# Performance work log

Hardware: AMD Instinct MI355X
Metric: run time of the kernel (lower is better)

Reference implementation:

```python
import jax, jax.numpy as jnp
import numpy as np

V, D, B, L = 100000, 64, 4096, 200

def setup_inputs() -> dict:
    key = jax.random.key(0)
    ks = jax.random.split(key, 10)
    s = 0.05  # keep activations in a sane range for sigmoid
    return {
        "item_ids": jax.random.randint(ks[0], (B,), 0, V),
        "history": jax.random.randint(ks[1], (B, L), 0, V),
        "hist_len": jax.random.randint(ks[2], (B,), 1, L + 1),
        "emb_table": jax.random.normal(ks[3], (V, D), jnp.float32) * s,
        "aW1": jax.random.normal(ks[4], (3 * D, D), jnp.float32) * s,
        "ab1": jnp.zeros((D,), jnp.float32),
        "aW2": jax.random.normal(ks[5], (D, 1), jnp.float32) * s,
        "ab2": jnp.zeros((1,), jnp.float32),
        "fW1": jax.random.normal(ks[6], (3 * D, 128), jnp.float32) * s,
        "fb1": jnp.zeros((128,), jnp.float32),
        "fW2": jax.random.normal(ks[7], (128, 64), jnp.float32) * s,
        "fb2": jnp.zeros((64,), jnp.float32),
        "fW3": jax.random.normal(ks[8], (64, 1), jnp.float32) * s,
        "fb3": jnp.zeros((1,), jnp.float32),
    }

def reference(item_ids, history, hist_len, emb_table, aW1, ab1, aW2, ab2,
              fW1, fb1, fW2, fb2, fW3, fb3):
    target = emb_table[item_ids]                      # [B, D]
    hist = emb_table[history]                         # [B, L, D]
    # original pads short histories with zero rows -> zero the padded tail
    mask = (jnp.arange(hist.shape[1])[None, :] < hist_len[:, None]).astype(hist.dtype)
    hist = hist * mask[..., None]
    tgt = jnp.broadcast_to(target[:, None, :], hist.shape)     # [B, L, D]
    # attention_fc takes 3*D features: (hist, target, hist*target)
    feat = jnp.concatenate([hist, tgt, hist * tgt], axis=-1)   # [B, L, 3D]
    h = jax.nn.relu(feat @ aW1 + ab1)                 # [B, L, D]
    scores = (h @ aW2 + ab2)[..., 0]                  # [B, L]
    # faithful to original: softmax over full padded length (no length mask)
    w = jax.nn.softmax(scores, axis=1)
    pooled = jnp.einsum('bl,bld->bd', w, hist)        # [B, D]
    comb = jnp.concatenate([target, pooled, pooled - target], axis=-1)  # [B, 3D]
    z = jax.nn.relu(comb @ fW1 + fb1)
    z = jax.nn.relu(z @ fW2 + fb2)
    return jax.nn.sigmoid(z @ fW3 + fb3)              # [B, 1]
```

## Files before the change

### kernel.cpp

```cpp
#include <hip/hip_runtime.h>
#include <hip/hip_bf16.h>

#define NV 100000
#define ND 64
#define NB 4096
#define NL 200
#define MT 13

typedef __bf16 bf16_t;
typedef __bf16 bf16x8 __attribute__((ext_vector_type(8)));
typedef float f32x4 __attribute__((ext_vector_type(4)));

#define TB_ELEMS ((long)NV * ND)

__global__ __launch_bounds__(256)
void cvt_kernel(const float* __restrict__ emb, bf16_t* __restrict__ tb)
{
    long i = ((long)blockIdx.x * 256 + threadIdx.x) * 8;
    if (i < TB_ELEMS) {
        f32x4 a0 = *(const f32x4*)(emb + i);
        f32x4 a1 = *(const f32x4*)(emb + i + 4);
        bf16x8 o;
#pragma unroll
        for (int j = 0; j < 4; ++j) { o[j] = (bf16_t)a0[j]; o[j + 4] = (bf16_t)a1[j]; }
        *(bf16x8*)(tb + i) = o;
    }
}

__global__ __launch_bounds__(256)
void din_kernel1(const int* __restrict__ item_ids,
                 const int* __restrict__ history,
                 const int* __restrict__ hist_len,
                 const float* __restrict__ emb,
                 const bf16_t* __restrict__ tb,
                 const float* __restrict__ aW1,
                 const float* __restrict__ ab1,
                 const float* __restrict__ aW2,
                 float* __restrict__ comb_ws)
{
    __shared__ __align__(16) bf16_t histA[208 * 64];
    __shared__ __align__(16) bf16_t wbT[64 * 64];
    __shared__ float tgt[64];
    __shared__ float cb[64];
    __shared__ __align__(16) float scores[208];
    __shared__ float wts[208];
    __shared__ float pp[4 * 64];
    __shared__ float red[8];
    __shared__ float pooled[64];

    const int b   = blockIdx.x;
    const int tid = threadIdx.x;
    const int len = hist_len[b];

    if (tid < 64) tgt[tid] = emb[(long)item_ids[b] * ND + tid];

    {
        const int p  = tid & 1;
        const int l0 = tid >> 1;
        const int l1 = l0 + 128;
        const bf16x8 z = (bf16x8)(bf16_t)0.f;
        bf16x8 v00 = z, v01 = z, v02 = z, v03 = z;
        bf16x8 v10 = z, v11 = z, v12 = z, v13 = z;
        if (l0 < len) {
            const bf16_t* s = tb + (long)history[(long)b * NL + l0] * ND + p * 32;
            v00 = *(const bf16x8*)(s);
            v01 = *(const bf16x8*)(s + 8);
            v02 = *(const bf16x8*)(s + 16);
            v03 = *(const bf16x8*)(s + 24);
        }
        if (l1 < len) {
            const bf16_t* s = tb + (long)history[(long)b * NL + l1] * ND + p * 32;
            v10 = *(const bf16x8*)(s);
            v11 = *(const bf16x8*)(s + 8);
            v12 = *(const bf16x8*)(s + 16);
            v13 = *(const bf16x8*)(s + 24);
        }
        {
            bf16_t* d = &histA[l0 * 64];
            const int S = (l0 & 7) << 3;
            *(bf16x8*)&d[(p * 32 +  0) ^ S] = v00;
            *(bf16x8*)&d[(p * 32 +  8) ^ S] = v01;
            *(bf16x8*)&d[(p * 32 + 16) ^ S] = v02;
            *(bf16x8*)&d[(p * 32 + 24) ^ S] = v03;
        }
        if (l1 < 208) {
            bf16_t* d = &histA[l1 * 64];
            const int S = (l1 & 7) << 3;
            *(bf16x8*)&d[(p * 32 +  0) ^ S] = v10;
            *(bf16x8*)&d[(p * 32 +  8) ^ S] = v11;
            *(bf16x8*)&d[(p * 32 + 16) ^ S] = v12;
            *(bf16x8*)&d[(p * 32 + 24) ^ S] = v13;
        }
    }
    __syncthreads();

    {
        const int n  = tid & 63;
        const int kp = tid >> 6;
        float csum = 0.f;
        bf16x8 w0, w1;
#pragma unroll
        for (int i = 0; i < 16; ++i) {
            int k = kp * 16 + i;
            float tk = tgt[k];
            float w  = aW1[k * 64 + n] + tk * aW1[(128 + k) * 64 + n];
            if (i < 8) w0[i] = (bf16_t)w; else w1[i - 8] = (bf16_t)w;
            csum += tk * aW1[(64 + k) * 64 + n];
        }
        const int S = (n & 7) << 3;
        *(bf16x8*)&wbT[n * 64 + ((kp * 16    ) ^ S)] = w0;
        *(bf16x8*)&wbT[n * 64 + ((kp * 16 + 8) ^ S)] = w1;
        pp[kp * 64 + n] = csum;
    }
    __syncthreads();
    if (tid < 64) cb[tid] = ab1[tid] + pp[tid] + pp[64 + tid] + pp[128 + tid] + pp[192 + tid];
    __syncthreads();

    {
        const int wave = tid >> 6;
        const int lane = tid & 63;
        const int col  = lane & 15;
        const int quad = lane >> 4;

        bf16x8 bfrag[4][2];
#pragma unroll
        for (int nt = 0; nt < 4; ++nt) {
            const int n = nt * 16 + col;
            const int S = (n & 7) << 3;
#pragma unroll
            for (int kb = 0; kb < 2; ++kb)
                bfrag[nt][kb] = *(const bf16x8*)&wbT[n * 64 + ((kb * 32 + quad * 8) ^ S)];
        }
        float cvals[4], a2vals[4];
#pragma unroll
        for (int nt = 0; nt < 4; ++nt) {
            cvals[nt]  = cb[nt * 16 + col];
            a2vals[nt] = aW2[nt * 16 + col];
        }

        for (int mt = wave; mt < MT; mt += 4) {
            const int row = mt * 16 + col;
            const int S   = (row & 7) << 3;
            const bf16_t* base = &histA[row * 64];
            bf16x8 af0 = *(const bf16x8*)&base[(     quad * 8) ^ S];
            bf16x8 af1 = *(const bf16x8*)&base[(32 + quad * 8) ^ S];
            float sc[4] = {0.f, 0.f, 0.f, 0.f};
#pragma unroll
            for (int nt = 0; nt < 4; ++nt) {
                f32x4 acc = {0.f, 0.f, 0.f, 0.f};
                acc = __builtin_amdgcn_mfma_f32_16x16x32_bf16(af0, bfrag[nt][0], acc, 0, 0, 0);
                acc = __builtin_amdgcn_mfma_f32_16x16x32_bf16(af1, bfrag[nt][1], acc, 0, 0, 0);
#pragma unroll
                for (int i = 0; i < 4; ++i) {
                    float h = acc[i] + cvals[nt];
                    h = h > 0.f ? h : 0.f;
                    sc[i] += h * a2vals[nt];
                }
            }
            for (int off = 1; off < 16; off <<= 1)
#pragma unroll
                for (int i = 0; i < 4; ++i)
                    sc[i] += __shfl_xor(sc[i], off, 64);
            if (col == 0) {
                f32x4 outv = {sc[0], sc[1], sc[2], sc[3]};
                *(f32x4*)&scores[mt * 16 + quad * 4] = outv;
            }
        }
    }
    __syncthreads();

    {
        float s = (tid < NL) ? scores[tid] : -1e30f;
        float m = s;
        for (int off = 32; off > 0; off >>= 1) m = fmaxf(m, __shfl_xor(m, off, 64));
        if ((tid & 63) == 0) red[tid >> 6] = m;
        __syncthreads();
        m = fmaxf(fmaxf(red[0], red[1]), fmaxf(red[2], red[3]));
        float e = (tid < NL) ? __expf(s - m) : 0.f;
        float ssum = e;
        for (int off = 32; off > 0; off >>= 1) ssum += __shfl_xor(ssum, off, 64);
        if ((tid & 63) == 0) red[4 + (tid >> 6)] = ssum;
        __syncthreads();
        float tot = red[4] + red[5] + red[6] + red[7];
        if (tid < NL) wts[tid] = e / tot;
    }
    __syncthreads();

    {
        const int wave = tid >> 6, lane = tid & 63;
        float acc = 0.f;
        for (int i = 0; i < 50; ++i) {
            int l = wave * 50 + i;
            float wl = wts[l];
            acc += wl * (float)histA[l * 64 + (lane ^ ((l & 7) << 3))];
        }
        pp[wave * 64 + lane] = acc;
    }
    __syncthreads();
    if (tid < 64) pooled[tid] = pp[tid] + pp[64 + tid] + pp[128 + tid] + pp[192 + tid];
    __syncthreads();

    if (tid < 192) {
        float v;
        if (tid < 64)       v = tgt[tid];
        else if (tid < 128) v = pooled[tid - 64];
        else                v = pooled[tid - 128] - tgt[tid - 128];
        comb_ws[(long)b * 192 + tid] = v;
    }
}

__global__ __launch_bounds__(256)
void din_kernel2(const float* __restrict__ comb,
                 const float* __restrict__ fW1, const float* __restrict__ fb1,
                 const float* __restrict__ fW2, const float* __restrict__ fb2,
                 const float* __restrict__ fW3, const float* __restrict__ fb3,
                 float* __restrict__ out)
{
    __shared__ float z1s[16 * 130];
    __shared__ float z2s[16 * 66];
    const int tid = threadIdx.x;
    const int r   = tid >> 4;
    const int c   = tid & 15;
    const int row = blockIdx.x * 16 + r;

    float acc[8];
    for (int jj = 0; jj < 8; ++jj) acc[jj] = fb1[c * 8 + jj];
    for (int i = 0; i < 192; ++i) {
        float cm = comb[(long)row * 192 + i];
        const float* wr = fW1 + i * 128 + c * 8;
        f32x4 w0 = *(const f32x4*)(wr);
        f32x4 w1 = *(const f32x4*)(wr + 4);
        for (int jj = 0; jj < 4; ++jj) {
            acc[jj]     += cm * w0[jj];
            acc[jj + 4] += cm * w1[jj];
        }
    }
    for (int jj = 0; jj < 8; ++jj) z1s[r * 130 + c * 8 + jj] = fmaxf(acc[jj], 0.f);
    __syncthreads();

    float a2[4];
    for (int jj = 0; jj < 4; ++jj) a2[jj] = fb2[c * 4 + jj];
    for (int i = 0; i < 128; ++i) {
        float zv = z1s[r * 130 + i];
        f32x4 w = *(const f32x4*)(fW2 + i * 64 + c * 4);
        for (int jj = 0; jj < 4; ++jj) a2[jj] += zv * w[jj];
    }
    for (int jj = 0; jj < 4; ++jj) z2s[r * 66 + c * 4 + jj] = fmaxf(a2[jj], 0.f);
    __syncthreads();

    if (c == 0) {
        float s = fb3[0];
        for (int j = 0; j < 64; ++j) s += z2s[r * 66 + j] * fW3[j];
        out[row] = 1.f / (1.f + __expf(-s));
    }
}

extern "C" void kernel_launch(void* const* d_in, const int* in_sizes, int n_in,
                              void* d_out, int out_size, void* d_ws, size_t ws_size,
                              hipStream_t stream) {
    const int*   item_ids = (const int*)d_in[0];
    const int*   history  = (const int*)d_in[1];
    const int*   hist_len = (const int*)d_in[2];
    const float* emb      = (const float*)d_in[3];
    const float* aW1      = (const float*)d_in[4];
    const float* ab1      = (const float*)d_in[5];
    const float* aW2      = (const float*)d_in[6];
    const float* fW1      = (const float*)d_in[8];
    const float* fb1      = (const float*)d_in[9];
    const float* fW2      = (const float*)d_in[10];
    const float* fb2      = (const float*)d_in[11];
    const float* fW3      = (const float*)d_in[12];
    const float* fb3      = (const float*)d_in[13];

    bf16_t* tb   = (bf16_t*)d_ws;
    float*  comb = (float*)((char*)d_ws + (size_t)(TB_ELEMS * 2));

    cvt_kernel<<<(int)(TB_ELEMS / 8 / 256 + 1), 256, 0, stream>>>(emb, tb);
    din_kernel1<<<NB, 256, 0, stream>>>(item_ids, history, hist_len, emb, tb,
                                        aW1, ab1, aW2, comb);
    din_kernel2<<<NB / 16, 256, 0, stream>>>(comb, fW1, fb1, fW2, fb2, fW3, fb3,
                                             (float*)d_out);
}
```

Measured before the change: 163.0 us.

## Fuse final MLP into attention kernel and drop first barrier

Moves the three-layer output MLP into the per-sample attention kernel, computing it per block with split-K partial sums in reused shared memory. This removes the second kernel launch and the global round-trip of the combined feature buffer. It also reads the target embedding directly from global memory in the weight-folding step so one __syncthreads can be dropped, and adds a launch-bounds occupancy hint of 4 blocks. The cost is that each of the 4096 blocks now re-reads the MLP weights, and the hint may constrain registers.

```diff
diff --git a/kernel.cpp b/kernel.cpp
--- a/kernel.cpp
+++ b/kernel.cpp
@@ -27,7 +27,7 @@
     }
 }
 
-__global__ __launch_bounds__(256)
+__global__ __launch_bounds__(256, 4)
 void din_kernel1(const int* __restrict__ item_ids,
                  const int* __restrict__ history,
                  const int* __restrict__ hist_len,
@@ -36,7 +36,10 @@
                  const float* __restrict__ aW1,
                  const float* __restrict__ ab1,
                  const float* __restrict__ aW2,
-                 float* __restrict__ comb_ws)
+                 const float* __restrict__ fW1, const float* __restrict__ fb1,
+                 const float* __restrict__ fW2, const float* __restrict__ fb2,
+                 const float* __restrict__ fW3, const float* __restrict__ fb3,
+                 float* __restrict__ out)
 {
     __shared__ __align__(16) bf16_t histA[208 * 64];
     __shared__ __align__(16) bf16_t wbT[64 * 64];
@@ -47,6 +50,11 @@
     __shared__ float pp[4 * 64];
     __shared__ float red[8];
     __shared__ float pooled[64];
+
+    float* mlp_pp = (float*)wbT;
+    float* z1     = (float*)wbT + 1024;
+    float* z2     = (float*)wbT + 1152;
+    float* comb_l = scores;
 
     const int b   = blockIdx.x;
     const int tid = threadIdx.x;
@@ -92,17 +100,17 @@
             *(bf16x8*)&d[(p * 32 + 24) ^ S] = v13;
         }
     }
-    __syncthreads();
-
-    {
-        const int n  = tid & 63;
-        const int kp = tid >> 6;
+
+    {
+        const int n    = tid & 63;
+        const int kp   = tid >> 6;
+        const long trow = (long)item_ids[b] * ND;
         float csum = 0.f;
         bf16x8 w0, w1;
 #pragma unroll
         for (int i = 0; i < 16; ++i) {
             int k = kp * 16 + i;
-            float tk = tgt[k];
+            float tk = emb[trow + k];
             float w  = aW1[k * 64 + n] + tk * aW1[(128 + k) * 64 + n];
             if (i < 8) w0[i] = (bf16_t)w; else w1[i - 8] = (bf16_t)w;
             csum += tk * aW1[(64 + k) * 64 + n];
@@ -205,53 +213,60 @@
         if (tid < 64)       v = tgt[tid];
         else if (tid < 128) v = pooled[tid - 64];
         else                v = pooled[tid - 128] - tgt[tid - 128];
-        comb_ws[(long)b * 192 + tid] = v;
-    }
-}
-
-__global__ __launch_bounds__(256)
-void din_kernel2(const float* __restrict__ comb,
-                 const float* __restrict__ fW1, const float* __restrict__ fb1,
-                 const float* __restrict__ fW2, const float* __restrict__ fb2,
-                 const float* __restrict__ fW3, const float* __restrict__ fb3,
-                 float* __restrict__ out)
-{
-    __shared__ float z1s[16 * 130];
-    __shared__ float z2s[16 * 66];
-    const int tid = threadIdx.x;
-    const int r   = tid >> 4;
-    const int c   = tid & 15;
-    const int row = blockIdx.x * 16 + r;
-
-    float acc[8];
-    for (int jj = 0; jj < 8; ++jj) acc[jj] = fb1[c * 8 + jj];
-    for (int i = 0; i < 192; ++i) {
-        float cm = comb[(long)row * 192 + i];
-        const float* wr = fW1 + i * 128 + c * 8;
-        f32x4 w0 = *(const f32x4*)(wr);
-        f32x4 w1 = *(const f32x4*)(wr + 4);
-        for (int jj = 0; jj < 4; ++jj) {
-            acc[jj]     += cm * w0[jj];
-            acc[jj + 4] += cm * w1[jj];
-        }
-    }
-    for (int jj = 0; jj < 8; ++jj) z1s[r * 130 + c * 8 + jj] = fmaxf(acc[jj], 0.f);
-    __syncthreads();
-
-    float a2[4];
-    for (int jj = 0; jj < 4; ++jj) a2[jj] = fb2[c * 4 + jj];
-    for (int i = 0; i < 128; ++i) {
-        float zv = z1s[r * 130 + i];
-        f32x4 w = *(const f32x4*)(fW2 + i * 64 + c * 4);
-        for (int jj = 0; jj < 4; ++jj) a2[jj] += zv * w[jj];
-    }
-    for (int jj = 0; jj < 4; ++jj) z2s[r * 66 + c * 4 + jj] = fmaxf(a2[jj], 0.f);
-    __syncthreads();
-
-    if (c == 0) {
-        float s = fb3[0];
-        for (int j = 0; j < 64; ++j) s += z2s[r * 66 + j] * fW3[j];
-        out[row] = 1.f / (1.f + __expf(-s));
+        comb_l[tid] = v;
+    }
+    __syncthreads();
+
+    {
+        const int c = tid & 31;
+        const int g = tid >> 5;
+        f32x4 acc = {0.f, 0.f, 0.f, 0.f};
+#pragma unroll
+        for (int ii = 0; ii < 24; ++ii) {
+            int i = g * 24 + ii;
+            float cm = comb_l[i];
+            f32x4 w = *(const f32x4*)(fW1 + (long)i * 128 + c * 4);
+#pragma unroll
+            for (int jj = 0; jj < 4; ++jj) acc[jj] += cm * w[jj];
+        }
+        *(f32x4*)&mlp_pp[g * 128 + c * 4] = acc;
+    }
+    __syncthreads();
+    if (tid < 128) {
+        float s = fb1[tid];
+#pragma unroll
+        for (int g = 0; g < 8; ++g) s += mlp_pp[g * 128 + tid];
+        z1[tid] = fmaxf(s, 0.f);
+    }
+    __syncthreads();
+
+    {
+        const int c = tid & 15;
+        const int g = tid >> 4;
+        f32x4 acc = {0.f, 0.f, 0.f, 0.f};
+#pragma unroll
+        for (int ii = 0; ii < 8; ++ii) {
+            int i = g * 8 + ii;
+            float zv = z1[i];
+            f32x4 w = *(const f32x4*)(fW2 + (long)i * 64 + c * 4);
+#pragma unroll
+            for (int jj = 0; jj < 4; ++jj) acc[jj] += zv * w[jj];
+        }
+        *(f32x4*)&mlp_pp[g * 64 + c * 4] = acc;
+    }
+    __syncthreads();
+    if (tid < 64) {
+        float s = fb2[tid];
+#pragma unroll
+        for (int g = 0; g < 16; ++g) s += mlp_pp[g * 64 + tid];
+        z2[tid] = fmaxf(s, 0.f);
+    }
+    __syncthreads();
+
+    if (tid < 64) {
+        float s = z2[tid] * fW3[tid];
+        for (int off = 32; off > 0; off >>= 1) s += __shfl_xor(s, off, 64);
+        if (tid == 0) out[b] = 1.f / (1.f + __expf(-(s + fb3[0])));
     }
 }
 
@@ -272,12 +287,11 @@
     const float* fW3      = (const float*)d_in[12];
     const float* fb3      = (const float*)d_in[13];
 
-    bf16_t* tb   = (bf16_t*)d_ws;
-    float*  comb = (float*)((char*)d_ws + (size_t)(TB_ELEMS * 2));
+    bf16_t* tb = (bf16_t*)d_ws;
 
     cvt_kernel<<<(int)(TB_ELEMS / 8 / 256 + 1), 256, 0, stream>>>(emb, tb);
     din_kernel1<<<NB, 256, 0, stream>>>(item_ids, history, hist_len, emb, tb,
-                                        aW1, ab1, aW2, comb);
-    din_kernel2<<<NB / 16, 256, 0, stream>>>(comb, fW1, fb1, fW2, fb2, fW3, fb3,
-                                             (float*)d_out);
+                                        aW1, ab1, aW2,
+                                        fW1, fb1, fW2, fb2, fW3, fb3,
+                                        (float*)d_out);
 }
```

Result: faster. 149.8 us (-8.1%).
